# Kernel tuning notes

Hardware: AMD Instinct MI355X
Metric: run time of the kernel (lower is better)

## Reference

```python
import jax, jax.numpy as jnp
import numpy as np

MAX_DIS = 15
PCD_RANGE = np.array([0.0, 0.0, 0.0, 30.0, 30.0, 14.0])
VOXEL = np.array([2.0, 2.0, 2.0])


def _make_locs():
    low, high = PCD_RANGE[:3], PCD_RANGE[3:]
    grid = ((high - low) // VOXEL + 1).astype(int)  # [16,16,8]
    axes = [low[i] + np.arange(grid[i]) * VOXEL[i] for i in range(3)]
    locs = np.stack(np.meshgrid(*axes, indexing='ij'), axis=-1).reshape(-1, 3)
    return jnp.asarray(locs, jnp.float32)  # [L=2048, 3]


def setup_inputs() -> dict:
    key = jax.random.key(0)
    low, high = PCD_RANGE[:3], PCD_RANGE[3:]
    pcd = jax.random.uniform(key, (4, 8192, 3), dtype=jnp.float32)
    pcd = pcd * jnp.asarray(high - low, jnp.float32) + jnp.asarray(low, jnp.float32)
    return {"pcd": pcd, "locs": _make_locs()}


def reference(pcd, locs):
    # pcd: [B, N, 3]; locs: [L, 3]
    # dis[l, b, n] = ceil(||pcd[b,n] - locs[l]||)
    diff = pcd[None, :, :, :] - locs[:, None, None, :]      # [L, B, N, 3]
    dis = jnp.ceil(jnp.sqrt(jnp.sum(diff * diff, axis=-1)))  # [L, B, N]
    # cumulative distance-threshold counts: feature[t] = #{n : dis <= t+1}
    feats = [jnp.where(dis <= jnp.float32(t + 1), 1.0, 0.0).sum(axis=-1)
             for t in range(MAX_DIS)]                        # each [L, B]
    feature = jnp.stack(feats, axis=0)                       # [MAX_DIS, L, B]
    return feature.transpose(2, 1, 0)                        # [B, L, MAX_DIS]
```

## Files before the change

### kernel.cpp

```cpp
#include <hip/hip_runtime.h>


#define BATCH 4
#define NPTS 8192
#define NLOC 2048
#define NT 15
#define SPLITS 64
#define LOCS_PER_BLOCK 4
#define PPS (NPTS / SPLITS)

#if __has_builtin(__builtin_amdgcn_sqrtf)
#define FAST_SQRT(x) __builtin_amdgcn_sqrtf(x)
#else
#define FAST_SQRT(x) sqrtf(x)
#endif

__global__ __launch_bounds__(256) void manual_feature_kernel(
    const float* __restrict__ pcd, const float* __restrict__ locs,
    float* __restrict__ out)
{
    const int tid   = threadIdx.x;
    const int li    = tid & (LOCS_PER_BLOCK - 1);
    const int split = tid >> 2;
    const int b     = blockIdx.x >> 9;
    const int ltile = blockIdx.x & 511;
    const int loc   = ltile * LOCS_PER_BLOCK + li;

    const float lx = locs[loc * 3 + 0];
    const float ly = locs[loc * 3 + 1];
    const float lz = locs[loc * 3 + 2];

    unsigned int h2[4] = {0u, 0u, 0u, 0u};

    const float4* base =
        reinterpret_cast<const float4*>(pcd + (size_t)(b * NPTS + split * PPS) * 3);

#pragma unroll 4
    for (int bt = 0; bt < PPS / 8; ++bt) {
        const float4 f0 = base[bt * 6 + 0];
        const float4 f1 = base[bt * 6 + 1];
        const float4 f2 = base[bt * 6 + 2];
        const float4 f3 = base[bt * 6 + 3];
        const float4 f4 = base[bt * 6 + 4];
        const float4 f5 = base[bt * 6 + 5];

        unsigned long long acc0 = 0ull, acc1 = 0ull;
        {
            float dx, dy, dz, d2, d;
            unsigned int f;
#define DO_POINT(A, PX, PY, PZ)                                     \
            dx = (PX) - lx; dy = (PY) - ly; dz = (PZ) - lz;         \
            d2 = dx * dx + dy * dy + dz * dz;                       \
            d  = FAST_SQRT(d2);                                     \
            f  = (unsigned int)d;                                   \
            f  = (f < 15u) ? f : 15u;                               \
            A += 1ull << (4u * f);

            DO_POINT(acc0, f0.x, f0.y, f0.z)
            DO_POINT(acc1, f0.w, f1.x, f1.y)
            DO_POINT(acc0, f1.z, f1.w, f2.x)
            DO_POINT(acc1, f2.y, f2.z, f2.w)
            DO_POINT(acc0, f3.x, f3.y, f3.z)
            DO_POINT(acc1, f3.w, f4.x, f4.y)
            DO_POINT(acc0, f4.z, f4.w, f5.x)
            DO_POINT(acc1, f5.y, f5.z, f5.w)
#undef DO_POINT
        }
        const unsigned long long acc = acc0 + acc1;
        const unsigned int lo = (unsigned int)acc;
        const unsigned int hi = (unsigned int)(acc >> 32);
        h2[0] += lo & 0x0F0F0F0Fu;
        h2[1] += (lo >> 4) & 0x0F0F0F0Fu;
        h2[2] += hi & 0x0F0F0F0Fu;
        h2[3] += (hi >> 4) & 0x0F0F0F0Fu;
    }

    unsigned int h[16];
#pragma unroll
    for (int j = 0; j < 16; ++j) {
        const unsigned int word = h2[(j & 1) + ((j >> 3) << 1)];
        h[j] = (word >> (8 * ((j >> 1) & 3))) & 0xFFu;
    }

    __shared__ int part[256][17];
    unsigned int p = 0;
#pragma unroll
    for (int t = 0; t < NT; ++t) { p += h[t]; part[tid][t] = (int)p; }
    __syncthreads();

    if (tid < LOCS_PER_BLOCK * NT) {
        const int li2 = tid / NT;
        const int t   = tid - li2 * NT;
        int s = 0;
#pragma unroll
        for (int k = 0; k < SPLITS; ++k)
            s += part[k * LOCS_PER_BLOCK + li2][t];
        out[((size_t)b * NLOC + (size_t)(ltile * LOCS_PER_BLOCK + li2)) * NT + t] =
            (float)s;
    }
}

extern "C" void kernel_launch(void* const* d_in, const int* in_sizes, int n_in,
                              void* d_out, int out_size, void* d_ws, size_t ws_size,
                              hipStream_t stream) {
    const float* pcd  = (const float*)d_in[0];
    const float* locs = (const float*)d_in[1];
    float* out = (float*)d_out;
    manual_feature_kernel<<<dim3(BATCH * (NLOC / LOCS_PER_BLOCK)), dim3(256), 0,
                            stream>>>(pcd, locs, out);
}
```

Measured before the change: 30.22 us.

## Transpose point cloud to SoA and use packed float2 math per wave-location

Adds a pre-pass kernel that converts the AoS point cloud into separate X/Y/Z arrays in workspace. The main kernel then gives each wavefront one location (made wave-uniform with readfirstlane) and has lanes read coalesced float4s, computing distances in packed two-wide float vectors. The aim is better load coalescing, scalar location values and packed FP32 arithmetic, at the cost of an extra kernel launch and a workspace round trip. If the workspace is too small, it falls back to the old kernel.

```diff
diff --git a/kernel.cpp b/kernel.cpp
--- a/kernel.cpp
+++ b/kernel.cpp
@@ -5,9 +5,8 @@
 #define NPTS 8192
 #define NLOC 2048
 #define NT 15
-#define SPLITS 64
-#define LOCS_PER_BLOCK 4
-#define PPS (NPTS / SPLITS)
+
+typedef float v2f __attribute__((ext_vector_type(2)));
 
 #if __has_builtin(__builtin_amdgcn_sqrtf)
 #define FAST_SQRT(x) __builtin_amdgcn_sqrtf(x)
@@ -15,7 +14,114 @@
 #define FAST_SQRT(x) sqrtf(x)
 #endif
 
-__global__ __launch_bounds__(256) void manual_feature_kernel(
+__global__ __launch_bounds__(256) void transpose_kernel(
+    const float* __restrict__ pcd, float* __restrict__ X,
+    float* __restrict__ Y, float* __restrict__ Z)
+{
+    const int g = blockIdx.x * 256 + threadIdx.x;
+    const float4* p = reinterpret_cast<const float4*>(pcd) + (size_t)g * 3;
+    const float4 f0 = p[0], f1 = p[1], f2 = p[2];
+    reinterpret_cast<float4*>(X)[g] = make_float4(f0.x, f0.w, f1.z, f2.y);
+    reinterpret_cast<float4*>(Y)[g] = make_float4(f0.y, f1.x, f1.w, f2.z);
+    reinterpret_cast<float4*>(Z)[g] = make_float4(f0.z, f1.y, f2.x, f2.w);
+}
+
+__global__ __launch_bounds__(256, 8) void feature_soa_kernel(
+    const float* __restrict__ X, const float* __restrict__ Y,
+    const float* __restrict__ Z, const float* __restrict__ locs,
+    float* __restrict__ out)
+{
+    const int tid   = threadIdx.x;
+    const int lane  = tid & 63;
+    const int wv    = tid >> 6;
+    const int b     = blockIdx.x >> 9;
+    const int ltile = blockIdx.x & 511;
+    const int loc   = __builtin_amdgcn_readfirstlane(ltile * 4 + wv);
+
+    const float lx = locs[loc * 3 + 0];
+    const float ly = locs[loc * 3 + 1];
+    const float lz = locs[loc * 3 + 2];
+    const v2f nlx = {-lx, -lx};
+    const v2f nly = {-ly, -ly};
+    const v2f nlz = {-lz, -lz};
+
+    const float4* Xb = reinterpret_cast<const float4*>(X + (size_t)b * NPTS);
+    const float4* Yb = reinterpret_cast<const float4*>(Y + (size_t)b * NPTS);
+    const float4* Zb = reinterpret_cast<const float4*>(Z + (size_t)b * NPTS);
+
+    unsigned int h2[4] = {0u, 0u, 0u, 0u};
+
+    for (int bt = 0; bt < 16; ++bt) {
+        const int i0 = (bt * 2 + 0) * 64 + lane;
+        const int i1 = (bt * 2 + 1) * 64 + lane;
+        const float4 xa = Xb[i0], ya = Yb[i0], za = Zb[i0];
+        const float4 xc = Xb[i1], yc = Yb[i1], zc = Zb[i1];
+
+        unsigned long long acc0 = 0ull, acc1 = 0ull;
+#define DO_PAIR(A, X01, Y01, Z01)                                   \
+        {                                                           \
+            const v2f dx = (X01) + nlx;                             \
+            const v2f dy = (Y01) + nly;                             \
+            const v2f dz = (Z01) + nlz;                             \
+            const v2f d2 = dx * dx + dy * dy + dz * dz;             \
+            unsigned int fa = (unsigned int)FAST_SQRT(d2.x);        \
+            unsigned int fb = (unsigned int)FAST_SQRT(d2.y);        \
+            fa = fa < 15u ? fa : 15u;                               \
+            fb = fb < 15u ? fb : 15u;                               \
+            A += 1ull << (fa << 2);                                 \
+            A += 1ull << (fb << 2);                                 \
+        }
+        {
+            const v2f x01 = {xa.x, xa.y}, y01 = {ya.x, ya.y}, z01 = {za.x, za.y};
+            const v2f x23 = {xa.z, xa.w}, y23 = {ya.z, ya.w}, z23 = {za.z, za.w};
+            DO_PAIR(acc0, x01, y01, z01)
+            DO_PAIR(acc1, x23, y23, z23)
+        }
+        {
+            const v2f x01 = {xc.x, xc.y}, y01 = {yc.x, yc.y}, z01 = {zc.x, zc.y};
+            const v2f x23 = {xc.z, xc.w}, y23 = {yc.z, yc.w}, z23 = {zc.z, zc.w};
+            DO_PAIR(acc0, x01, y01, z01)
+            DO_PAIR(acc1, x23, y23, z23)
+        }
+#undef DO_PAIR
+        const unsigned long long acc = acc0 + acc1;
+        const unsigned int lo = (unsigned int)acc;
+        const unsigned int hi = (unsigned int)(acc >> 32);
+        h2[0] += lo & 0x0F0F0F0Fu;
+        h2[1] += (lo >> 4) & 0x0F0F0F0Fu;
+        h2[2] += hi & 0x0F0F0F0Fu;
+        h2[3] += (hi >> 4) & 0x0F0F0F0Fu;
+    }
+
+    unsigned int h[16];
+#pragma unroll
+    for (int j = 0; j < 16; ++j) {
+        const unsigned int word = h2[(j & 1) + ((j >> 3) << 1)];
+        h[j] = (word >> (8 * ((j >> 1) & 3))) & 0xFFu;
+    }
+
+    __shared__ int part[256][17];
+    unsigned int p = 0;
+#pragma unroll
+    for (int t = 0; t < NT; ++t) { p += h[t]; part[tid][t] = (int)p; }
+    __syncthreads();
+
+    if (tid < 4 * NT) {
+        const int li2 = tid / NT;
+        const int t   = tid - li2 * NT;
+        int s = 0;
+#pragma unroll
+        for (int k = 0; k < 64; ++k)
+            s += part[li2 * 64 + k][t];
+        out[((size_t)b * NLOC + (size_t)(ltile * 4 + li2)) * NT + t] = (float)s;
+    }
+}
+
+#define SPLITS 64
+#define LOCS_PER_BLOCK 4
+#define PPS (NPTS / SPLITS)
+
+__global__ __launch_bounds__(256) void manual_feature_fallback(
     const float* __restrict__ pcd, const float* __restrict__ locs,
     float* __restrict__ out)
 {
@@ -31,7 +137,6 @@
     const float lz = locs[loc * 3 + 2];
 
     unsigned int h2[4] = {0u, 0u, 0u, 0u};
-
     const float4* base =
         reinterpret_cast<const float4*>(pcd + (size_t)(b * NPTS + split * PPS) * 3);
 
@@ -106,6 +211,18 @@
     const float* pcd  = (const float*)d_in[0];
     const float* locs = (const float*)d_in[1];
     float* out = (float*)d_out;
-    manual_feature_kernel<<<dim3(BATCH * (NLOC / LOCS_PER_BLOCK)), dim3(256), 0,
-                            stream>>>(pcd, locs, out);
-}
+
+    const size_t need = (size_t)BATCH * NPTS * 3 * sizeof(float);
+    if (ws_size >= need) {
+        float* X = (float*)d_ws;
+        float* Y = X + (size_t)BATCH * NPTS;
+        float* Z = Y + (size_t)BATCH * NPTS;
+        transpose_kernel<<<dim3(BATCH * NPTS / 4 / 256), dim3(256), 0, stream>>>(
+            pcd, X, Y, Z);
+        feature_soa_kernel<<<dim3(BATCH * (NLOC / 4)), dim3(256), 0, stream>>>(
+            X, Y, Z, locs, out);
+    } else {
+        manual_feature_fallback<<<dim3(BATCH * (NLOC / 4)), dim3(256), 0,
+                                  stream>>>(pcd, locs, out);
+    }
+}
```

Result: slower. 35.18 us (+16.4%).
